# Performance work log

Hardware: AMD Instinct MI355X
Metric: run time of the kernel (lower is better)

## Reference

```python
import jax, jax.numpy as jnp
import numpy as np

B, N, DIM = 4, 2048, 256
K = 16            # num_nearest_neighbors
EDGE_DIM = 2
M_DIM = 64
EIN = 2 * DIM + 1 + EDGE_DIM   # 515, edge_mlp input dim
VALID_RADIUS = 0.0
MASK_FILL = 1e5


def setup_inputs() -> dict:
    key = jax.random.key(0)
    ks = jax.random.split(key, 16)
    emb = jax.random.normal(ks[0], (B, N, DIM), dtype=jnp.float32)
    coors = jax.random.normal(ks[1], (B, N, 3), dtype=jnp.float32)
    adj = jax.random.bernoulli(ks[2], 0.004, (B, N, N))            # avg degree ~8
    feat = jax.random.normal(ks[3], (B, N, N, EDGE_DIM), dtype=jnp.float32)
    mask = jax.random.bernoulli(ks[4], 0.9, (B, N))
    s = 0.02
    eW1 = jax.random.normal(ks[5], (EIN, 2 * EIN), dtype=jnp.float32) * s
    eb1 = jnp.zeros((2 * EIN,), dtype=jnp.float32)
    eW2 = jax.random.normal(ks[6], (2 * EIN, M_DIM), dtype=jnp.float32) * s
    eb2 = jnp.zeros((M_DIM,), dtype=jnp.float32)
    nW1 = jax.random.normal(ks[7], (DIM + M_DIM, 2 * DIM), dtype=jnp.float32) * s
    nb1 = jnp.zeros((2 * DIM,), dtype=jnp.float32)
    nW2 = jax.random.normal(ks[8], (2 * DIM, DIM), dtype=jnp.float32) * s
    nb2 = jnp.zeros((DIM,), dtype=jnp.float32)
    return {"emb": emb, "coors": coors, "adj": adj, "feat": feat, "mask": mask,
            "eW1": eW1, "eb1": eb1, "eW2": eW2, "eb2": eb2,
            "nW1": nW1, "nb1": nb1, "nW2": nW2, "nb2": nb2}


def reference(emb, coors, adj, feat, mask, eW1, eb1, eW2, eb2, nW1, nb1, nW2, nb2):
    b, n, d = emb.shape
    # pairwise squared distances [b,n,n]
    rel = coors[:, :, None, :] - coors[:, None, :, :]
    rel_dist = jnp.sum(rel * rel, axis=-1)
    # ranking for kNN selection (masked pairs pushed far, self=-1, adjacent=0)
    rank_mask = mask[:, :, None] & mask[:, None, :]
    ranking = jnp.where(rank_mask, rel_dist, MASK_FILL)
    eye = jnp.eye(n, dtype=bool)[None]
    adj_ns = adj & ~eye
    ranking = jnp.where(eye, -1.0, ranking)
    ranking = jnp.where(adj_ns, 0.0, ranking)
    # k smallest
    neg_vals, idx = jax.lax.top_k(-ranking, K)          # idx [b,n,K]
    nbhd_ranking = -neg_vals
    nbhd_mask = nbhd_ranking <= VALID_RADIUS
    # gathers
    rel_dist_k = jnp.take_along_axis(rel_dist, idx, axis=2)[..., None]      # [b,n,K,1]
    edges_k = jnp.take_along_axis(feat, idx[..., None], axis=2)             # [b,n,K,E]
    feats_j = jax.vmap(lambda f, ix: f[ix])(emb, idx)                       # [b,n,K,d]
    feats_i = jnp.broadcast_to(emb[:, :, None, :], feats_j.shape)
    edge_input = jnp.concatenate([feats_i, feats_j, rel_dist_k, edges_k], axis=-1)
    # edge MLP: Linear -> SiLU -> Linear -> SiLU (dropout=0 in eval)
    h = jax.nn.silu(edge_input @ eW1 + eb1)
    m_ij = jax.nn.silu(h @ eW2 + eb2)                                       # [b,n,K,m]
    # pair mask
    mask_j = jax.vmap(lambda m, ix: m[ix])(mask, idx)                       # [b,n,K]
    pair_mask = (mask[:, :, None] & mask_j) & nbhd_mask
    m_ij = jnp.where(pair_mask[..., None], m_ij, 0.0)
    m_i = jnp.sum(m_ij, axis=2)                                             # [b,n,m]
    # node MLP with residual (norm_feats=False)
    node_in = jnp.concatenate([emb, m_i], axis=-1)
    node_out = jax.nn.silu(node_in @ nW1 + nb1) @ nW2 + nb2 + emb
    # update_coors=False -> coors unchanged; module returns full tuple
    return (node_out, coors, adj, feat, mask)
```

## Files before the change

### kernel.cpp

```cpp
#include <hip/hip_runtime.h>
#include <stdint.h>

typedef unsigned short ushort_t;

#define NN    2048
#define DIMC  256
#define H1    1030
#define MD    64
#define NROWS 8192

#define HP       1040

#define KPAD     1056
#define NKS      33

#define NPQ      2060
#define NPQP     2112
#define KN1      320
#define KN2      512

typedef __bf16 bf16x8 __attribute__((ext_vector_type(8)));
typedef float  f32x4  __attribute__((ext_vector_type(4)));
typedef ushort_t u16x8 __attribute__((ext_vector_type(8)));

__device__ __forceinline__ float bfu2f(ushort_t u){ union{unsigned u; float f;} v; v.u = ((unsigned)u)<<16; return v.f; }
__device__ __forceinline__ ushort_t f2bfu(float f){ union{float f; unsigned u;} v; v.f=f; unsigned r = (v.u + 0x7FFFu + ((v.u>>16)&1u))>>16; return (ushort_t)r; }
__device__ __forceinline__ float siluf(float x){ return x / (1.0f + __expf(-x)); }
__device__ __forceinline__ void split_hilo(float v, ushort_t& hi, ushort_t& lo){
    hi = f2bfu(v);
    lo = f2bfu(v - bfu2f(hi));
}

__global__ void adj_kernel(const int* __restrict__ adj, const int* __restrict__ mask,
                           float* __restrict__ out_adj, float* __restrict__ out_mask,
                           int* __restrict__ pairs, int* __restrict__ counter)
{
    const int w = threadIdx.x >> 6, lane = threadIdx.x & 63;
    const int row = blockIdx.x*4 + w;
    const int b = row >> 11, i = row & (NN-1);
    __shared__ int nbrs[4][15];
    int total = 0;
    const size_t rbase = (size_t)row * NN;
    const int4* arow = (const int4*)(adj + rbase);
    float4* orow = (float4*)(out_adj + rbase);
    for (int c = 0; c < NN/256; c++) {
        int4 v = arow[c*64 + lane];
        int j0 = c*256 + lane*4;
        float4 ov; ov.x = v.x?1.f:0.f; ov.y = v.y?1.f:0.f; ov.z = v.z?1.f:0.f; ov.w = v.w?1.f:0.f;
        orow[c*64 + lane] = ov;
        bool p0 = v.x && (j0   != i);
        bool p1 = v.y && (j0+1 != i);
        bool p2 = v.z && (j0+2 != i);
        bool p3 = v.w && (j0+3 != i);
        unsigned long long b0 = __ballot(p0), b1 = __ballot(p1), b2 = __ballot(p2), b3 = __ballot(p3);
        unsigned long long below = (1ull<<lane)-1ull;
        int slot = total + __popcll(b0&below)+__popcll(b1&below)+__popcll(b2&below)+__popcll(b3&below);
        if (p0 && slot < 15) nbrs[w][slot] = j0;
        slot += p0;
        if (p1 && slot < 15) nbrs[w][slot] = j0+1;
        slot += p1;
        if (p2 && slot < 15) nbrs[w][slot] = j0+2;
        slot += p2;
        if (p3 && slot < 15) nbrs[w][slot] = j0+3;
        total += __popcll(b0)+__popcll(b1)+__popcll(b2)+__popcll(b3);
    }
    int cnt = total < 15 ? total : 15;
    const int mv = mask[row];
    if (lane == 0) out_mask[row] = mv ? 1.0f : 0.0f;
    if (mv != 0) {
        int jl = (lane < cnt) ? nbrs[w][lane] : 0;
        bool ok = (lane < cnt) && (mask[b*NN + jl] != 0);
        unsigned long long bm = __ballot(ok);
        int npair = 1 + __popcll(bm);
        int basep = 0;
        if (lane == 0) basep = atomicAdd(counter, npair);
        basep = __shfl(basep, 0);
        if (lane == 0) pairs[basep] = (row << 16) | i;
        if (ok) {
            int pos = basep + 1 + __popcll(bm & ((1ull<<lane)-1ull));
            pairs[pos] = (row << 16) | jl;
        }
    }
}

template<int K>
__device__ __forceinline__ void mfma_tile2(const ushort_t* __restrict__ Ah, const ushort_t* __restrict__ Al, int sA,
                                           const ushort_t* __restrict__ Bh, const ushort_t* __restrict__ Bl, int sB,
                                           int lane, f32x4 (&acc)[2][4])
{
    const int m16 = lane & 15, kg = lane >> 4;
    const ushort_t* a0h = Ah + (size_t)m16*sA + kg*8;
    const ushort_t* a0l = Al + (size_t)m16*sA + kg*8;
    const ushort_t* a1h = a0h + (size_t)16*sA;
    const ushort_t* a1l = a0l + (size_t)16*sA;
    const ushort_t* brh = Bh + (size_t)m16*sB + kg*8;
    const ushort_t* brl = Bl + (size_t)m16*sB + kg*8;
#pragma unroll 4
    for (int ks = 0; ks < K/32; ks++) {
        bf16x8 a0h_ = *reinterpret_cast<const bf16x8*>(a0h + ks*32);
        bf16x8 a0l_ = *reinterpret_cast<const bf16x8*>(a0l + ks*32);
        bf16x8 a1h_ = *reinterpret_cast<const bf16x8*>(a1h + ks*32);
        bf16x8 a1l_ = *reinterpret_cast<const bf16x8*>(a1l + ks*32);
#pragma unroll
        for (int nf = 0; nf < 4; nf++) {
            bf16x8 bh = *reinterpret_cast<const bf16x8*>(brh + (size_t)(nf*16)*sB + ks*32);
            bf16x8 bl = *reinterpret_cast<const bf16x8*>(brl + (size_t)(nf*16)*sB + ks*32);
            acc[0][nf] = __builtin_amdgcn_mfma_f32_16x16x32_bf16(a0h_, bh, acc[0][nf], 0, 0, 0);
            acc[0][nf] = __builtin_amdgcn_mfma_f32_16x16x32_bf16(a0h_, bl, acc[0][nf], 0, 0, 0);
            acc[0][nf] = __builtin_amdgcn_mfma_f32_16x16x32_bf16(a0l_, bh, acc[0][nf], 0, 0, 0);
            acc[1][nf] = __builtin_amdgcn_mfma_f32_16x16x32_bf16(a1h_, bh, acc[1][nf], 0, 0, 0);
            acc[1][nf] = __builtin_amdgcn_mfma_f32_16x16x32_bf16(a1h_, bl, acc[1][nf], 0, 0, 0);
            acc[1][nf] = __builtin_amdgcn_mfma_f32_16x16x32_bf16(a1l_, bh, acc[1][nf], 0, 0, 0);
        }
    }
}

__global__ void prep_weights(const float* __restrict__ eW1, const float* __restrict__ nW1,
                             const float* __restrict__ nW2, const float* __restrict__ eW2,
                             const float* __restrict__ emb,
                             ushort_t* __restrict__ Wpq_h, ushort_t* __restrict__ Wpq_l,
                             ushort_t* __restrict__ W1T_h, ushort_t* __restrict__ W1T_l,
                             ushort_t* __restrict__ NW2T_h, ushort_t* __restrict__ NW2T_l,
                             ushort_t* __restrict__ W2T, float* __restrict__ wt4,
                             ushort_t* __restrict__ Ah, ushort_t* __restrict__ Al)
{
    int t = blockIdx.x*256 + threadIdx.x;
    if (t < NPQP*DIMC) {
        int n = t >> 8, k = t & 255;
        float v = 0.f;
        if (n < H1) v = eW1[(size_t)k*H1 + n];
        else if (n < NPQ) v = eW1[(size_t)(256+k)*H1 + (n - H1)];
        ushort_t hi, lo; split_hilo(v, hi, lo);
        Wpq_h[t] = hi; Wpq_l[t] = lo;
        return;
    }
    t -= NPQP*DIMC;
    if (t < 512*KN1) {
        int n = t / KN1, k = t - n*KN1;
        ushort_t hi, lo; split_hilo(nW1[(size_t)k*512 + n], hi, lo);
        W1T_h[t] = hi; W1T_l[t] = lo;
        return;
    }
    t -= 512*KN1;
    if (t < 256*KN2) {
        int n = t >> 9, k = t & 511;
        ushort_t hi, lo; split_hilo(nW2[(size_t)k*256 + n], hi, lo);
        NW2T_h[t] = hi; NW2T_l[t] = lo;
        return;
    }
    t -= 256*KN2;
    if (t < MD*KPAD) {
        int n = t / KPAD, k = t - n*KPAD;
        W2T[t] = f2bfu((k < H1) ? eW2[(size_t)k*MD + n] : 0.0f);
        return;
    }
    t -= MD*KPAD;
    if (t < 3*HP) {
        int c = t / HP, k = t - c*HP;
        wt4[t] = (k < H1) ? eW1[(size_t)(512+c)*H1 + k] : 0.f;
        return;
    }
    t -= 3*HP;
    if (t < NROWS*DIMC) {
        int r = t >> 8, k = t & 255;
        ushort_t hi, lo; split_hilo(emb[t], hi, lo);
        Ah[(size_t)r*KN1 + k] = hi; Al[(size_t)r*KN1 + k] = lo;
    }
}

__global__ void prep_macc(const float* __restrict__ macc, ushort_t* __restrict__ Ah, ushort_t* __restrict__ Al){
    int t = blockIdx.x*256 + threadIdx.x;
    if (t >= NROWS*MD) return;
    int r = t >> 6, k = t & 63;
    ushort_t hi, lo; split_hilo(macc[t], hi, lo);
    Ah[(size_t)r*KN1 + DIMC + k] = hi; Al[(size_t)r*KN1 + DIMC + k] = lo;
}

__global__ __launch_bounds__(256)
void gemm_pq_mfma(const ushort_t* __restrict__ Aeph, const ushort_t* __restrict__ Aepl,
                  const ushort_t* __restrict__ Wh, const ushort_t* __restrict__ Wl,
                  const float* __restrict__ eb1,
                  ushort_t* __restrict__ Pb, ushort_t* __restrict__ Qb)
{
    const int lane = threadIdx.x & 63, w = threadIdx.x >> 6;
    const int rowBase = blockIdx.x*128 + w*32;
    const int colBase = blockIdx.y*64;
    f32x4 acc[2][4] = {{{0,0,0,0},{0,0,0,0},{0,0,0,0},{0,0,0,0}},
                       {{0,0,0,0},{0,0,0,0},{0,0,0,0},{0,0,0,0}}};
    mfma_tile2<DIMC>(Aeph + (size_t)rowBase*KN1, Aepl + (size_t)rowBase*KN1, KN1,
                     Wh + (size_t)colBase*DIMC, Wl + (size_t)colBase*DIMC, DIMC, lane, acc);
    const int m16 = lane & 15, kg = lane >> 4;
#pragma unroll
    for (int tt = 0; tt < 2; tt++) {
#pragma unroll
        for (int nf = 0; nf < 4; nf++) {
#pragma unroll
            for (int r = 0; r < 4; r++) {
                int row = rowBase + tt*16 + kg*4 + r;
                int n = colBase + nf*16 + m16;
                if (n < H1) {
                    Pb[(size_t)row*HP + n] = f2bfu(acc[tt][nf][r] + eb1[n]);
                } else if (n < NPQ) {
                    Qb[(size_t)row*HP + (n - H1)] = f2bfu(acc[tt][nf][r]);
                }
            }
        }
    }
}

__global__ __launch_bounds__(256)
void node1_mfma(const ushort_t* __restrict__ Aeph, const ushort_t* __restrict__ Aepl,
                const ushort_t* __restrict__ W1h, const ushort_t* __restrict__ W1l,
                const float* __restrict__ nb1, ushort_t* __restrict__ Hh, ushort_t* __restrict__ Hl)
{
    const int lane = threadIdx.x & 63, w = threadIdx.x >> 6;
    const int rowBase = blockIdx.x*128 + w*32;
    const int colBase = blockIdx.y*64;
    f32x4 acc[2][4] = {{{0,0,0,0},{0,0,0,0},{0,0,0,0},{0,0,0,0}},
                       {{0,0,0,0},{0,0,0,0},{0,0,0,0},{0,0,0,0}}};
    mfma_tile2<KN1>(Aeph + (size_t)rowBase*KN1, Aepl + (size_t)rowBase*KN1, KN1,
                    W1h + (size_t)colBase*KN1, W1l + (size_t)colBase*KN1, KN1, lane, acc);
    const int m16 = lane & 15, kg = lane >> 4;
#pragma unroll
    for (int tt = 0; tt < 2; tt++) {
#pragma unroll
        for (int nf = 0; nf < 4; nf++) {
#pragma unroll
            for (int r = 0; r < 4; r++) {
                int row = rowBase + tt*16 + kg*4 + r;
                int col = colBase + nf*16 + m16;
                float s = siluf(acc[tt][nf][r] + nb1[col]);
                ushort_t hi, lo; split_hilo(s, hi, lo);
                Hh[(size_t)row*KN2 + col] = hi;
                Hl[(size_t)row*KN2 + col] = lo;
            }
        }
    }
}

__global__ __launch_bounds__(256)
void node2_mfma(const ushort_t* __restrict__ Hh, const ushort_t* __restrict__ Hl,
                const ushort_t* __restrict__ W2h, const ushort_t* __restrict__ W2l,
                const float* __restrict__ nb2, const float* __restrict__ emb,
                float* __restrict__ out_node)
{
    const int lane = threadIdx.x & 63, w = threadIdx.x >> 6;
    const int rowBase = blockIdx.x*128 + w*32;
    const int colBase = blockIdx.y*64;
    f32x4 acc[2][4] = {{{0,0,0,0},{0,0,0,0},{0,0,0,0},{0,0,0,0}},
                       {{0,0,0,0},{0,0,0,0},{0,0,0,0},{0,0,0,0}}};
    mfma_tile2<KN2>(Hh + (size_t)rowBase*KN2, Hl + (size_t)rowBase*KN2, KN2,
                    W2h + (size_t)colBase*KN2, W2l + (size_t)colBase*KN2, KN2, lane, acc);
    const int m16 = lane & 15, kg = lane >> 4;
#pragma unroll
    for (int tt = 0; tt < 2; tt++) {
#pragma unroll
        for (int nf = 0; nf < 4; nf++) {
#pragma unroll
            for (int r = 0; r < 4; r++) {
                int row = rowBase + tt*16 + kg*4 + r;
                int col = colBase + nf*16 + m16;
                size_t o = (size_t)row*DIMC + col;
                out_node[o] = acc[tt][nf][r] + nb2[col] + emb[o];
            }
        }
    }
}

__global__ __launch_bounds__(256)
void edge_mfma(const int* __restrict__ pairs, const int* __restrict__ counter,
               const ushort_t* __restrict__ P, const ushort_t* __restrict__ Q,
               const float* __restrict__ coors, const float* __restrict__ feat,
               const float* __restrict__ wt4,
               const ushort_t* __restrict__ W2T, const float* __restrict__ eb2,
               float* __restrict__ macc)
{
    const int np = counter[0];
    const int lane = threadIdx.x & 63;
    const int w = threadIdx.x >> 6;
    const int wbase = blockIdx.x*64 + w*16;
    if (wbase >= np) return;
    const int m16 = lane & 15, kg = lane >> 4;

    const int pidx = wbase + m16;
    const int e = pairs[(pidx < np) ? pidx : wbase];
    const int row = e >> 16, j = e & 0xFFFF;
    const int jr = ((row >> 11) << 11) + j;
    const float dx = coors[row*3+0] - coors[jr*3+0];
    const float dy = coors[row*3+1] - coors[jr*3+1];
    const float dz = coors[row*3+2] - coors[jr*3+2];
    const float d  = dx*dx + dy*dy + dz*dz;
    const size_t fo = ((size_t)row*NN + j)*2;
    const float f0 = feat[fo], f1 = feat[fo+1];
    const ushort_t* Prow = P + (size_t)row*HP;
    const ushort_t* Qrow = Q + (size_t)jr*HP;
    const float* w512 = wt4;
    const float* w513 = wt4 + HP;
    const float* w514 = wt4 + 2*HP;
    const int kb = kg*8;

    f32x4 acc[4] = {{0,0,0,0},{0,0,0,0},{0,0,0,0},{0,0,0,0}};

    for (int ks = 0; ks < NKS; ks++) {
        const int k0 = ks*32 + kb;
        u16x8 hv = {0,0,0,0,0,0,0,0};
        u16x8 lv = {0,0,0,0,0,0,0,0};
        if (k0 < H1) {
            u16x8 pv8 = *reinterpret_cast<const u16x8*>(Prow + k0);
            u16x8 qv8 = *reinterpret_cast<const u16x8*>(Qrow + k0);
            f32x4 wa0 = *reinterpret_cast<const f32x4*>(w512 + k0);
            f32x4 wa1 = *reinterpret_cast<const f32x4*>(w512 + k0 + 4);
            f32x4 wb0 = *reinterpret_cast<const f32x4*>(w513 + k0);
            f32x4 wb1 = *reinterpret_cast<const f32x4*>(w513 + k0 + 4);
            f32x4 wc0 = *reinterpret_cast<const f32x4*>(w514 + k0);
            f32x4 wc1 = *reinterpret_cast<const f32x4*>(w514 + k0 + 4);
#pragma unroll
            for (int ee = 0; ee < 8; ee++) {
                float va = (ee < 4) ? wa0[ee] : wa1[ee-4];
                float vb = (ee < 4) ? wb0[ee] : wb1[ee-4];
                float vc = (ee < 4) ? wc0[ee] : wc1[ee-4];
                float x = bfu2f(pv8[ee]) + bfu2f(qv8[ee]) + d*va + f0*vb + f1*vc;
                float h = (k0 + ee < H1) ? siluf(x) : 0.f;
                union {float f; unsigned u;} cv; cv.f = h;
                unsigned hib = cv.u & 0xFFFF0000u;
                hv[ee] = (ushort_t)(hib >> 16);
                union {unsigned u; float f;} hf; hf.u = hib;
                union {float f; unsigned u;} lw; lw.f = h - hf.f;
                lv[ee] = (ushort_t)(lw.u >> 16);
            }
        }
        bf16x8 ah = *reinterpret_cast<bf16x8*>(&hv);
        bf16x8 al = *reinterpret_cast<bf16x8*>(&lv);
        const ushort_t* Wk = W2T + k0;
#pragma unroll
        for (int nf = 0; nf < 4; nf++) {
            bf16x8 bfr = *reinterpret_cast<const bf16x8*>(Wk + (size_t)(nf*16 + m16)*KPAD);
            acc[nf] = __builtin_amdgcn_mfma_f32_16x16x32_bf16(ah, bfr, acc[nf], 0, 0, 0);
            acc[nf] = __builtin_amdgcn_mfma_f32_16x16x32_bf16(al, bfr, acc[nf], 0, 0, 0);
        }
    }

#pragma unroll
    for (int nf = 0; nf < 4; nf++) {
        const int n = nf*16 + m16;
        const float bias = eb2[n];
#pragma unroll
        for (int r = 0; r < 4; r++) {
            int pe = wbase + kg*4 + r;
            if (pe < np) {
                int rr = pairs[pe] >> 16;
                float m = siluf(acc[nf][r] + bias);
                atomicAdd(&macc[(size_t)rr*MD + n], m);
            }
        }
    }
}

extern "C" void kernel_launch(void* const* d_in, const int* in_sizes, int n_in,
                              void* d_out, int out_size, void* d_ws, size_t ws_size,
                              hipStream_t stream)
{
    const float* emb   = (const float*)d_in[0];
    const float* coors = (const float*)d_in[1];
    const int*   adj   = (const int*)d_in[2];
    const float* feat  = (const float*)d_in[3];
    const int*   mask  = (const int*)d_in[4];
    const float* eW1   = (const float*)d_in[5];
    const float* eb1   = (const float*)d_in[6];
    const float* eW2   = (const float*)d_in[7];
    const float* eb2   = (const float*)d_in[8];
    const float* nW1   = (const float*)d_in[9];
    const float* nb1   = (const float*)d_in[10];
    const float* nW2   = (const float*)d_in[11];
    const float* nb2   = (const float*)d_in[12];

    float* out       = (float*)d_out;
    float* out_node  = out;
    float* out_coors = out + 2097152;
    float* out_adj   = out + 2121728;
    float* out_feat  = out + 18898944;
    float* out_mask  = out + 52453376;

    char* ws = (char*)d_ws;
    int*      counter = (int*)(ws + 0);
    float*    macc    = (float*)(ws + 256);
    int*      pairs   = (int*)(ws + 2097408);
    ushort_t* Pbuf    = (ushort_t*)(ws + 2621696);
    float*    wt4     = (float*)(ws + 19661056);

    char* scr = (char*)out_feat;
    ushort_t* Aep_h = (ushort_t*)(scr + 0);
    ushort_t* Aep_l = (ushort_t*)(scr + 5242880);
    ushort_t* Wpq_h = (ushort_t*)(scr + 10485760);
    ushort_t* Wpq_l = (ushort_t*)(scr + 11567104);
    ushort_t* W1T_h = (ushort_t*)(scr + 12648448);
    ushort_t* W1T_l = (ushort_t*)(scr + 12976128);
    ushort_t* NW2T_h= (ushort_t*)(scr + 13303808);
    ushort_t* NW2T_l= (ushort_t*)(scr + 13565952);
    ushort_t* Hid_h = (ushort_t*)(scr + 13828096);
    ushort_t* Hid_l = (ushort_t*)(scr + 22216704);
    ushort_t* Qbuf  = (ushort_t*)(scr + 30605312);

    ushort_t* W2T = (ushort_t*)out_node;

    hipMemsetAsync(counter, 0, 256, stream);
    hipMemsetAsync(macc, 0, (size_t)NROWS*MD*sizeof(float), stream);

    hipMemcpyAsync(out_coors, coors, (size_t)24576*sizeof(float), hipMemcpyDeviceToDevice, stream);

    adj_kernel<<<NROWS/4, 256, 0, stream>>>(adj, mask, out_adj, out_mask, pairs, counter);

    {
        int tot = NPQP*DIMC + 512*KN1 + 256*KN2 + MD*KPAD + 3*HP + NROWS*DIMC;
        prep_weights<<<(tot + 255)/256, 256, 0, stream>>>(eW1, nW1, nW2, eW2, emb,
                                                          Wpq_h, Wpq_l, W1T_h, W1T_l,
                                                          NW2T_h, NW2T_l, W2T, wt4,
                                                          Aep_h, Aep_l);
    }

    gemm_pq_mfma<<<dim3(NROWS/128, NPQP/64), 256, 0, stream>>>(Aep_h, Aep_l, Wpq_h, Wpq_l, eb1, Pbuf, Qbuf);

    edge_mfma<<<2048, 256, 0, stream>>>(pairs, counter, Pbuf, Qbuf, coors, feat,
                                        wt4, W2T, eb2, macc);

    prep_macc<<<(NROWS*MD + 255)/256, 256, 0, stream>>>(macc, Aep_h, Aep_l);
    node1_mfma<<<dim3(NROWS/128, 512/64), 256, 0, stream>>>(Aep_h, Aep_l, W1T_h, W1T_l, nb1, Hid_h, Hid_l);
    node2_mfma<<<dim3(NROWS/128, DIMC/64), 256, 0, stream>>>(Hid_h, Hid_l, NW2T_h, NW2T_l, nb2, emb, out_node);

    hipMemcpyAsync(out_feat, feat, (size_t)33554432*sizeof(float), hipMemcpyDeviceToDevice, stream);
}
```

Before: 725.1 us.

## Merge prep kernels, fuse macc split into node1, and overlap feat copy with node2

The adjacency scan, weight prep, macc zeroing and coors copy are merged into one launch. The macc hi/lo split is folded into node1's MFMA loop, so the prep_macc kernel goes away. The 134MB feat copy becomes extra blocks of the node2 kernel so it can overlap with the GEMM. Hid and NW2T buffers move from out_feat scratch into the workspace so the feat copy can run alongside. The aim is to cut launch overhead and serialization, at the cost of a larger mixed-role grid.

```diff
diff --git a/kernel.cpp b/kernel.cpp
--- a/kernel.cpp
+++ b/kernel.cpp
@@ -18,6 +18,13 @@
 #define NPQP     2112
 #define KN1      320
 #define KN2      512
+
+#define ADJ_BLKS 2048
+#define PREP_TOT (NPQP*DIMC + 512*KN1 + 256*KN2 + MD*KPAD + 3*HP + NROWS*DIMC)
+#define MACCZ    (NROWS*MD/4)
+#define COORSZ   (24576/4)
+#define N2_BLKS  256
+#define FCOPY4   (33554432/4)
 
 typedef __bf16 bf16x8 __attribute__((ext_vector_type(8)));
 typedef float  f32x4  __attribute__((ext_vector_type(4)));
@@ -31,55 +38,122 @@
     lo = f2bfu(v - bfu2f(hi));
 }
 
-__global__ void adj_kernel(const int* __restrict__ adj, const int* __restrict__ mask,
-                           float* __restrict__ out_adj, float* __restrict__ out_mask,
-                           int* __restrict__ pairs, int* __restrict__ counter)
-{
-    const int w = threadIdx.x >> 6, lane = threadIdx.x & 63;
-    const int row = blockIdx.x*4 + w;
-    const int b = row >> 11, i = row & (NN-1);
-    __shared__ int nbrs[4][15];
-    int total = 0;
-    const size_t rbase = (size_t)row * NN;
-    const int4* arow = (const int4*)(adj + rbase);
-    float4* orow = (float4*)(out_adj + rbase);
-    for (int c = 0; c < NN/256; c++) {
-        int4 v = arow[c*64 + lane];
-        int j0 = c*256 + lane*4;
-        float4 ov; ov.x = v.x?1.f:0.f; ov.y = v.y?1.f:0.f; ov.z = v.z?1.f:0.f; ov.w = v.w?1.f:0.f;
-        orow[c*64 + lane] = ov;
-        bool p0 = v.x && (j0   != i);
-        bool p1 = v.y && (j0+1 != i);
-        bool p2 = v.z && (j0+2 != i);
-        bool p3 = v.w && (j0+3 != i);
-        unsigned long long b0 = __ballot(p0), b1 = __ballot(p1), b2 = __ballot(p2), b3 = __ballot(p3);
-        unsigned long long below = (1ull<<lane)-1ull;
-        int slot = total + __popcll(b0&below)+__popcll(b1&below)+__popcll(b2&below)+__popcll(b3&below);
-        if (p0 && slot < 15) nbrs[w][slot] = j0;
-        slot += p0;
-        if (p1 && slot < 15) nbrs[w][slot] = j0+1;
-        slot += p1;
-        if (p2 && slot < 15) nbrs[w][slot] = j0+2;
-        slot += p2;
-        if (p3 && slot < 15) nbrs[w][slot] = j0+3;
-        total += __popcll(b0)+__popcll(b1)+__popcll(b2)+__popcll(b3);
-    }
-    int cnt = total < 15 ? total : 15;
-    const int mv = mask[row];
-    if (lane == 0) out_mask[row] = mv ? 1.0f : 0.0f;
-    if (mv != 0) {
-        int jl = (lane < cnt) ? nbrs[w][lane] : 0;
-        bool ok = (lane < cnt) && (mask[b*NN + jl] != 0);
-        unsigned long long bm = __ballot(ok);
-        int npair = 1 + __popcll(bm);
-        int basep = 0;
-        if (lane == 0) basep = atomicAdd(counter, npair);
-        basep = __shfl(basep, 0);
-        if (lane == 0) pairs[basep] = (row << 16) | i;
-        if (ok) {
-            int pos = basep + 1 + __popcll(bm & ((1ull<<lane)-1ull));
-            pairs[pos] = (row << 16) | jl;
-        }
+__global__ void stage1(const int* __restrict__ adj, const int* __restrict__ mask,
+                       const float* __restrict__ coors,
+                       const float* __restrict__ eW1, const float* __restrict__ nW1,
+                       const float* __restrict__ nW2, const float* __restrict__ eW2,
+                       const float* __restrict__ emb,
+                       float* __restrict__ out_adj, float* __restrict__ out_mask,
+                       float* __restrict__ out_coors,
+                       int* __restrict__ pairs, int* __restrict__ counter,
+                       ushort_t* __restrict__ Wpq_h, ushort_t* __restrict__ Wpq_l,
+                       ushort_t* __restrict__ W1T_h, ushort_t* __restrict__ W1T_l,
+                       ushort_t* __restrict__ NW2T_h, ushort_t* __restrict__ NW2T_l,
+                       ushort_t* __restrict__ W2T, float* __restrict__ wt4,
+                       ushort_t* __restrict__ Ah, ushort_t* __restrict__ Al,
+                       float* __restrict__ macc)
+{
+    if (blockIdx.x < ADJ_BLKS) {
+        const int w = threadIdx.x >> 6, lane = threadIdx.x & 63;
+        const int row = blockIdx.x*4 + w;
+        const int b = row >> 11, i = row & (NN-1);
+        __shared__ int nbrs[4][15];
+        int total = 0;
+        const size_t rbase = (size_t)row * NN;
+        const int4* arow = (const int4*)(adj + rbase);
+        float4* orow = (float4*)(out_adj + rbase);
+        for (int c = 0; c < NN/256; c++) {
+            int4 v = arow[c*64 + lane];
+            int j0 = c*256 + lane*4;
+            float4 ov; ov.x = v.x?1.f:0.f; ov.y = v.y?1.f:0.f; ov.z = v.z?1.f:0.f; ov.w = v.w?1.f:0.f;
+            orow[c*64 + lane] = ov;
+            bool p0 = v.x && (j0   != i);
+            bool p1 = v.y && (j0+1 != i);
+            bool p2 = v.z && (j0+2 != i);
+            bool p3 = v.w && (j0+3 != i);
+            unsigned long long b0 = __ballot(p0), b1 = __ballot(p1), b2 = __ballot(p2), b3 = __ballot(p3);
+            unsigned long long below = (1ull<<lane)-1ull;
+            int slot = total + __popcll(b0&below)+__popcll(b1&below)+__popcll(b2&below)+__popcll(b3&below);
+            if (p0 && slot < 15) nbrs[w][slot] = j0;
+            slot += p0;
+            if (p1 && slot < 15) nbrs[w][slot] = j0+1;
+            slot += p1;
+            if (p2 && slot < 15) nbrs[w][slot] = j0+2;
+            slot += p2;
+            if (p3 && slot < 15) nbrs[w][slot] = j0+3;
+            total += __popcll(b0)+__popcll(b1)+__popcll(b2)+__popcll(b3);
+        }
+        int cnt = total < 15 ? total : 15;
+        const int mv = mask[row];
+        if (lane == 0) out_mask[row] = mv ? 1.0f : 0.0f;
+        if (mv != 0) {
+            int jl = (lane < cnt) ? nbrs[w][lane] : 0;
+            bool ok = (lane < cnt) && (mask[b*NN + jl] != 0);
+            unsigned long long bm = __ballot(ok);
+            int npair = 1 + __popcll(bm);
+            int basep = 0;
+            if (lane == 0) basep = atomicAdd(counter, npair);
+            basep = __shfl(basep, 0);
+            if (lane == 0) pairs[basep] = (row << 16) | i;
+            if (ok) {
+                int pos = basep + 1 + __popcll(bm & ((1ull<<lane)-1ull));
+                pairs[pos] = (row << 16) | jl;
+            }
+        }
+        return;
+    }
+    int t = (blockIdx.x - ADJ_BLKS)*256 + threadIdx.x;
+    if (t < NPQP*DIMC) {
+        int n = t >> 8, k = t & 255;
+        float v = 0.f;
+        if (n < H1) v = eW1[(size_t)k*H1 + n];
+        else if (n < NPQ) v = eW1[(size_t)(256+k)*H1 + (n - H1)];
+        ushort_t hi, lo; split_hilo(v, hi, lo);
+        Wpq_h[t] = hi; Wpq_l[t] = lo;
+        return;
+    }
+    t -= NPQP*DIMC;
+    if (t < 512*KN1) {
+        int n = t / KN1, k = t - n*KN1;
+        ushort_t hi, lo; split_hilo(nW1[(size_t)k*512 + n], hi, lo);
+        W1T_h[t] = hi; W1T_l[t] = lo;
+        return;
+    }
+    t -= 512*KN1;
+    if (t < 256*KN2) {
+        int n = t >> 9, k = t & 511;
+        ushort_t hi, lo; split_hilo(nW2[(size_t)k*256 + n], hi, lo);
+        NW2T_h[t] = hi; NW2T_l[t] = lo;
+        return;
+    }
+    t -= 256*KN2;
+    if (t < MD*KPAD) {
+        int n = t / KPAD, k = t - n*KPAD;
+        W2T[t] = f2bfu((k < H1) ? eW2[(size_t)k*MD + n] : 0.0f);
+        return;
+    }
+    t -= MD*KPAD;
+    if (t < 3*HP) {
+        int c = t / HP, k = t - c*HP;
+        wt4[t] = (k < H1) ? eW1[(size_t)(512+c)*H1 + k] : 0.f;
+        return;
+    }
+    t -= 3*HP;
+    if (t < NROWS*DIMC) {
+        int r = t >> 8, k = t & 255;
+        ushort_t hi, lo; split_hilo(emb[t], hi, lo);
+        Ah[(size_t)r*KN1 + k] = hi; Al[(size_t)r*KN1 + k] = lo;
+        return;
+    }
+    t -= NROWS*DIMC;
+    if (t < MACCZ) {
+        float4 z; z.x = z.y = z.z = z.w = 0.f;
+        ((float4*)macc)[t] = z;
+        return;
+    }
+    t -= MACCZ;
+    if (t < COORSZ) {
+        ((float4*)out_coors)[t] = ((const float4*)coors)[t];
     }
 }
 
@@ -115,67 +189,6 @@
     }
 }
 
-__global__ void prep_weights(const float* __restrict__ eW1, const float* __restrict__ nW1,
-                             const float* __restrict__ nW2, const float* __restrict__ eW2,
-                             const float* __restrict__ emb,
-                             ushort_t* __restrict__ Wpq_h, ushort_t* __restrict__ Wpq_l,
-                             ushort_t* __restrict__ W1T_h, ushort_t* __restrict__ W1T_l,
-                             ushort_t* __restrict__ NW2T_h, ushort_t* __restrict__ NW2T_l,
-                             ushort_t* __restrict__ W2T, float* __restrict__ wt4,
-                             ushort_t* __restrict__ Ah, ushort_t* __restrict__ Al)
-{
-    int t = blockIdx.x*256 + threadIdx.x;
-    if (t < NPQP*DIMC) {
-        int n = t >> 8, k = t & 255;
-        float v = 0.f;
-        if (n < H1) v = eW1[(size_t)k*H1 + n];
-        else if (n < NPQ) v = eW1[(size_t)(256+k)*H1 + (n - H1)];
-        ushort_t hi, lo; split_hilo(v, hi, lo);
-        Wpq_h[t] = hi; Wpq_l[t] = lo;
-        return;
-    }
-    t -= NPQP*DIMC;
-    if (t < 512*KN1) {
-        int n = t / KN1, k = t - n*KN1;
-        ushort_t hi, lo; split_hilo(nW1[(size_t)k*512 + n], hi, lo);
-        W1T_h[t] = hi; W1T_l[t] = lo;
-        return;
-    }
-    t -= 512*KN1;
-    if (t < 256*KN2) {
-        int n = t >> 9, k = t & 511;
-        ushort_t hi, lo; split_hilo(nW2[(size_t)k*256 + n], hi, lo);
-        NW2T_h[t] = hi; NW2T_l[t] = lo;
-        return;
-    }
-    t -= 256*KN2;
-    if (t < MD*KPAD) {
-        int n = t / KPAD, k = t - n*KPAD;
-        W2T[t] = f2bfu((k < H1) ? eW2[(size_t)k*MD + n] : 0.0f);
-        return;
-    }
-    t -= MD*KPAD;
-    if (t < 3*HP) {
-        int c = t / HP, k = t - c*HP;
-        wt4[t] = (k < H1) ? eW1[(size_t)(512+c)*H1 + k] : 0.f;
-        return;
-    }
-    t -= 3*HP;
-    if (t < NROWS*DIMC) {
-        int r = t >> 8, k = t & 255;
-        ushort_t hi, lo; split_hilo(emb[t], hi, lo);
-        Ah[(size_t)r*KN1 + k] = hi; Al[(size_t)r*KN1 + k] = lo;
-    }
-}
-
-__global__ void prep_macc(const float* __restrict__ macc, ushort_t* __restrict__ Ah, ushort_t* __restrict__ Al){
-    int t = blockIdx.x*256 + threadIdx.x;
-    if (t >= NROWS*MD) return;
-    int r = t >> 6, k = t & 63;
-    ushort_t hi, lo; split_hilo(macc[t], hi, lo);
-    Ah[(size_t)r*KN1 + DIMC + k] = hi; Al[(size_t)r*KN1 + DIMC + k] = lo;
-}
-
 __global__ __launch_bounds__(256)
 void gemm_pq_mfma(const ushort_t* __restrict__ Aeph, const ushort_t* __restrict__ Aepl,
                   const ushort_t* __restrict__ Wh, const ushort_t* __restrict__ Wl,
@@ -211,6 +224,7 @@
 __global__ __launch_bounds__(256)
 void node1_mfma(const ushort_t* __restrict__ Aeph, const ushort_t* __restrict__ Aepl,
                 const ushort_t* __restrict__ W1h, const ushort_t* __restrict__ W1l,
+                const float* __restrict__ macc,
                 const float* __restrict__ nb1, ushort_t* __restrict__ Hh, ushort_t* __restrict__ Hl)
 {
     const int lane = threadIdx.x & 63, w = threadIdx.x >> 6;
@@ -218,9 +232,45 @@
     const int colBase = blockIdx.y*64;
     f32x4 acc[2][4] = {{{0,0,0,0},{0,0,0,0},{0,0,0,0},{0,0,0,0}},
                        {{0,0,0,0},{0,0,0,0},{0,0,0,0},{0,0,0,0}}};
-    mfma_tile2<KN1>(Aeph + (size_t)rowBase*KN1, Aepl + (size_t)rowBase*KN1, KN1,
-                    W1h + (size_t)colBase*KN1, W1l + (size_t)colBase*KN1, KN1, lane, acc);
+    mfma_tile2<DIMC>(Aeph + (size_t)rowBase*KN1, Aepl + (size_t)rowBase*KN1, KN1,
+                     W1h + (size_t)colBase*KN1, W1l + (size_t)colBase*KN1, KN1, lane, acc);
     const int m16 = lane & 15, kg = lane >> 4;
+    {
+        const float* mr0 = macc + (size_t)(rowBase + m16)*MD;
+        const float* mr1 = macc + (size_t)(rowBase + 16 + m16)*MD;
+        const ushort_t* brh_b = W1h + ((size_t)colBase + m16)*KN1 + DIMC + kg*8;
+        const ushort_t* brl_b = W1l + ((size_t)colBase + m16)*KN1 + DIMC + kg*8;
+#pragma unroll
+        for (int ks = 0; ks < 2; ks++) {
+            int kk = ks*32 + kg*8;
+            f32x4 va = *reinterpret_cast<const f32x4*>(mr0 + kk);
+            f32x4 vb = *reinterpret_cast<const f32x4*>(mr0 + kk + 4);
+            f32x4 vc = *reinterpret_cast<const f32x4*>(mr1 + kk);
+            f32x4 vd = *reinterpret_cast<const f32x4*>(mr1 + kk + 4);
+            u16x8 h0, l0, h1, l1;
+#pragma unroll
+            for (int e = 0; e < 8; e++) {
+                ushort_t hi, lo;
+                split_hilo((e < 4) ? va[e] : vb[e-4], hi, lo); h0[e] = hi; l0[e] = lo;
+                split_hilo((e < 4) ? vc[e] : vd[e-4], hi, lo); h1[e] = hi; l1[e] = lo;
+            }
+            bf16x8 a0h = *reinterpret_cast<bf16x8*>(&h0);
+            bf16x8 a0l = *reinterpret_cast<bf16x8*>(&l0);
+            bf16x8 a1h = *reinterpret_cast<bf16x8*>(&h1);
+            bf16x8 a1l = *reinterpret_cast<bf16x8*>(&l1);
+#pragma unroll
+            for (int nf = 0; nf < 4; nf++) {
+                bf16x8 bh = *reinterpret_cast<const bf16x8*>(brh_b + (size_t)(nf*16)*KN1 + ks*32);
+                bf16x8 bl = *reinterpret_cast<const bf16x8*>(brl_b + (size_t)(nf*16)*KN1 + ks*32);
+                acc[0][nf] = __builtin_amdgcn_mfma_f32_16x16x32_bf16(a0h, bh, acc[0][nf], 0, 0, 0);
+                acc[0][nf] = __builtin_amdgcn_mfma_f32_16x16x32_bf16(a0h, bl, acc[0][nf], 0, 0, 0);
+                acc[0][nf] = __builtin_amdgcn_mfma_f32_16x16x32_bf16(a0l, bh, acc[0][nf], 0, 0, 0);
+                acc[1][nf] = __builtin_amdgcn_mfma_f32_16x16x32_bf16(a1h, bh, acc[1][nf], 0, 0, 0);
+                acc[1][nf] = __builtin_amdgcn_mfma_f32_16x16x32_bf16(a1h, bl, acc[1][nf], 0, 0, 0);
+                acc[1][nf] = __builtin_amdgcn_mfma_f32_16x16x32_bf16(a1l, bh, acc[1][nf], 0, 0, 0);
+            }
+        }
+    }
 #pragma unroll
     for (int tt = 0; tt < 2; tt++) {
 #pragma unroll
@@ -239,14 +289,21 @@
 }
 
 __global__ __launch_bounds__(256)
-void node2_mfma(const ushort_t* __restrict__ Hh, const ushort_t* __restrict__ Hl,
-                const ushort_t* __restrict__ W2h, const ushort_t* __restrict__ W2l,
-                const float* __restrict__ nb2, const float* __restrict__ emb,
-                float* __restrict__ out_node)
-{
+void stage5(const ushort_t* __restrict__ Hh, const ushort_t* __restrict__ Hl,
+            const ushort_t* __restrict__ W2h, const ushort_t* __restrict__ W2l,
+            const float* __restrict__ nb2, const float* __restrict__ emb,
+            const float* __restrict__ feat,
+            float* __restrict__ out_node, float* __restrict__ out_feat)
+{
+    if (blockIdx.x >= N2_BLKS) {
+        int t = (blockIdx.x - N2_BLKS)*256 + threadIdx.x;
+        if (t < FCOPY4) ((float4*)out_feat)[t] = ((const float4*)feat)[t];
+        return;
+    }
+    const int rb = blockIdx.x & 63, cb = blockIdx.x >> 6;
     const int lane = threadIdx.x & 63, w = threadIdx.x >> 6;
-    const int rowBase = blockIdx.x*128 + w*32;
-    const int colBase = blockIdx.y*64;
+    const int rowBase = rb*128 + w*32;
+    const int colBase = cb*64;
     f32x4 acc[2][4] = {{{0,0,0,0},{0,0,0,0},{0,0,0,0},{0,0,0,0}},
                        {{0,0,0,0},{0,0,0,0},{0,0,0,0},{0,0,0,0}}};
     mfma_tile2<KN2>(Hh + (size_t)rowBase*KN2, Hl + (size_t)rowBase*KN2, KN2,
@@ -387,6 +444,10 @@
     int*      pairs   = (int*)(ws + 2097408);
     ushort_t* Pbuf    = (ushort_t*)(ws + 2621696);
     float*    wt4     = (float*)(ws + 19661056);
+    ushort_t* Hid_h   = (ushort_t*)(ws + 19673536);
+    ushort_t* Hid_l   = (ushort_t*)(ws + 28062144);
+    ushort_t* NW2T_h  = (ushort_t*)(ws + 36450752);
+    ushort_t* NW2T_l  = (ushort_t*)(ws + 36712896);
 
     char* scr = (char*)out_feat;
     ushort_t* Aep_h = (ushort_t*)(scr + 0);
@@ -395,27 +456,18 @@
     ushort_t* Wpq_l = (ushort_t*)(scr + 11567104);
     ushort_t* W1T_h = (ushort_t*)(scr + 12648448);
     ushort_t* W1T_l = (ushort_t*)(scr + 12976128);
-    ushort_t* NW2T_h= (ushort_t*)(scr + 13303808);
-    ushort_t* NW2T_l= (ushort_t*)(scr + 13565952);
-    ushort_t* Hid_h = (ushort_t*)(scr + 13828096);
-    ushort_t* Hid_l = (ushort_t*)(scr + 22216704);
-    ushort_t* Qbuf  = (ushort_t*)(scr + 30605312);
+    ushort_t* Qbuf  = (ushort_t*)(scr + 13303808);
 
     ushort_t* W2T = (ushort_t*)out_node;
 
     hipMemsetAsync(counter, 0, 256, stream);
-    hipMemsetAsync(macc, 0, (size_t)NROWS*MD*sizeof(float), stream);
-
-    hipMemcpyAsync(out_coors, coors, (size_t)24576*sizeof(float), hipMemcpyDeviceToDevice, stream);
-
-    adj_kernel<<<NROWS/4, 256, 0, stream>>>(adj, mask, out_adj, out_mask, pairs, counter);
 
     {
-        int tot = NPQP*DIMC + 512*KN1 + 256*KN2 + MD*KPAD + 3*HP + NROWS*DIMC;
-        prep_weights<<<(tot + 255)/256, 256, 0, stream>>>(eW1, nW1, nW2, eW2, emb,
-                                                          Wpq_h, Wpq_l, W1T_h, W1T_l,
-                                                          NW2T_h, NW2T_l, W2T, wt4,
-                                                          Aep_h, Aep_l);
+        int extra = (PREP_TOT + MACCZ + COORSZ + 255)/256;
+        stage1<<<ADJ_BLKS + extra, 256, 0, stream>>>(adj, mask, coors, eW1, nW1, nW2, eW2, emb,
+                                                     out_adj, out_mask, out_coors, pairs, counter,
+                                                     Wpq_h, Wpq_l, W1T_h, W1T_l, NW2T_h, NW2T_l,
+                                                     W2T, wt4, Aep_h, Aep_l, macc);
     }
 
     gemm_pq_mfma<<<dim3(NROWS/128, NPQP/64), 256, 0, stream>>>(Aep_h, Aep_l, Wpq_h, Wpq_l, eb1, Pbuf, Qbuf);
@@ -423,9 +475,8 @@
     edge_mfma<<<2048, 256, 0, stream>>>(pairs, counter, Pbuf, Qbuf, coors, feat,
                                         wt4, W2T, eb2, macc);
 
-    prep_macc<<<(NROWS*MD + 255)/256, 256, 0, stream>>>(macc, Aep_h, Aep_l);
-    node1_mfma<<<dim3(NROWS/128, 512/64), 256, 0, stream>>>(Aep_h, Aep_l, W1T_h, W1T_l, nb1, Hid_h, Hid_l);
-    node2_mfma<<<dim3(NROWS/128, DIMC/64), 256, 0, stream>>>(Hid_h, Hid_l, NW2T_h, NW2T_l, nb2, emb, out_node);
-
-    hipMemcpyAsync(out_feat, feat, (size_t)33554432*sizeof(float), hipMemcpyDeviceToDevice, stream);
-}
+    node1_mfma<<<dim3(NROWS/128, 512/64), 256, 0, stream>>>(Aep_h, Aep_l, W1T_h, W1T_l, macc, nb1, Hid_h, Hid_l);
+
+    stage5<<<N2_BLKS + FCOPY4/256, 256, 0, stream>>>(Hid_h, Hid_l, NW2T_h, NW2T_l, nb2, emb, feat,
+                                                     out_node, out_feat);
+}
```

Measured after the change: 698.4 us. 1.04x faster.
